# Kernel optimization log

Measured on AMD Instinct MI355X. Metric: run time of the kernel, lower is better.

The kernel has to match this reference:

```python
import jax, jax.numpy as jnp
import numpy as np

B, N, C = 16, 2048, 3           # images, proposals/image, classes (incl. background)
K = 100                         # num_detections kept per class
SCORE_THRESH = 0.05
NMS_THRESH = 0.5
MIN_ANGLE = 10.0                # process_box min width (self.min_angle)
WX, WW = 1.0, 1.0               # box_coder reg_weights
NEG = jnp.float32(-1e9)


def setup_inputs() -> dict:
    key = jax.random.key(0)
    k1, k2, k3, k4 = jax.random.split(key, 4)
    class_logit = jax.random.normal(k1, (B, N, C), jnp.float32)
    box_regression = jax.random.normal(k2, (B, N, 2 * C), jnp.float32) * 0.1
    starts = jax.random.uniform(k3, (B, N), dtype=jnp.float32) * 300.0
    widths = jax.random.uniform(k4, (B, N), dtype=jnp.float32) * 50.0 + 12.0
    proposal = jnp.stack([starts, starts + widths], axis=-1)  # [B,N,2] 1-D intervals
    return {"class_logit": class_logit, "box_regression": box_regression,
            "proposal": proposal, "image_shape": 360}


def _decode(delta, prop):
    w = prop[:, 1] - prop[:, 0]
    ctr = prop[:, 0] + 0.5 * w
    dx = delta[:, 0] / WX
    dw = jnp.minimum(delta[:, 1] / WW, 4.0)  # clamp like torchvision
    pc = dx * w + ctr
    pw = jnp.exp(dw) * w
    return jnp.stack([pc - 0.5 * pw, pc + 0.5 * pw], axis=-1)  # [N,2]


def _iou_1d(a, b):
    inter = jnp.maximum(0.0, jnp.minimum(a[:, None, 1], b[None, :, 1])
                        - jnp.maximum(a[:, None, 0], b[None, :, 0]))
    union = (a[:, None, 1] - a[:, None, 0]) + (b[None, :, 1] - b[None, :, 0]) - inter
    return inter / jnp.maximum(union, 1e-8)  # [Na,Nb]


def _infer_one_class(score, delta, prop, image_shape):
    # score [N], delta [N,2], prop [N,2] -> [K,3] (start, end, score); invalid slots score=NEG
    box = _decode(delta, prop)
    lo = jnp.clip(box[:, 0], 0.0, image_shape)
    hi = jnp.clip(box[:, 1], 0.0, image_shape)
    box = jnp.stack([lo, hi], axis=-1)
    valid = ((hi - lo) >= MIN_ANGLE) & (score >= SCORE_THRESH)
    ms = jnp.where(valid, score, NEG)
    order = jnp.argsort(-ms)
    b = box[order]
    s = ms[order]
    sup = jax.lax.stop_gradient(_iou_1d(b, b)) > NMS_THRESH  # [N,N] bool
    idx = jnp.arange(N)

    def body(keep, i):  # greedy NMS in score order
        kill = sup[i] & keep[i] & (idx > i)
        return keep & ~kill, None

    keep0 = s > 0.5 * NEG
    keep, _ = jax.lax.scan(body, keep0, idx)
    ks = jnp.where(keep, s, NEG)
    top_s, top_i = jax.lax.top_k(ks, K)
    top_b = b[top_i]
    return jnp.concatenate([top_b, top_s[:, None]], axis=-1)  # [K,3]


def reference(class_logit, box_regression, proposal, image_shape):
    img = jnp.float32(image_shape)
    scores = jax.nn.softmax(class_logit, axis=-1)[..., 1:]        # [B,N,C-1] fg classes
    deltas = box_regression.reshape(B, N, C, 2)[:, :, 1:]         # [B,N,C-1,2]
    scores = jnp.moveaxis(scores, -1, 1)                          # [B,C-1,N]
    deltas = jnp.moveaxis(deltas, 2, 1)                           # [B,C-1,N,2]
    f = jax.vmap(jax.vmap(_infer_one_class, in_axes=(0, 0, None, None)),
                 in_axes=(0, 0, 0, None))
    return f(scores, deltas, proposal, img)  # [B, C-1, K, 3]
```

## Files before the change

kernel.cpp:

```cpp
#include <hip/hip_runtime.h>
#include <math.h>

#define B_IMG 16
#define N_PROP 2048
#define C_CLS 3
#define K_OUT 100
#define NTHREADS 1024
#define NWAVES (NTHREADS / 64)
#define NBLK64 (N_PROP / 64)

__device__ __forceinline__ unsigned long long shfl_xor_u64(unsigned long long v, int lx) {
    unsigned int lo = (unsigned int)__shfl_xor((int)(unsigned int)(v & 0xffffffffull), lx, 64);
    unsigned int hi = (unsigned int)__shfl_xor((int)(unsigned int)(v >> 32), lx, 64);
    return ((unsigned long long)hi << 32) | (unsigned long long)lo;
}
__device__ __forceinline__ float readlane_f(float v, int l) {
    return __int_as_float(__builtin_amdgcn_readlane(__float_as_int(v), l));
}
__device__ __forceinline__ unsigned long long readlane_u64(unsigned long long v, int l) {
    unsigned int lo = (unsigned int)__builtin_amdgcn_readlane((int)(unsigned int)(v & 0xffffffffull), l);
    unsigned int hi = (unsigned int)__builtin_amdgcn_readlane((int)(unsigned int)(v >> 32), l);
    return ((unsigned long long)hi << 32) | (unsigned long long)lo;
}
__device__ __forceinline__ bool iou_gt_half(float inter, float uni) {
    double b = (double)fmaxf(uni, 1e-8f);
    return (double)inter * 2.0 > b * 0x1.000001p0;
}
__device__ __forceinline__ float parse_imgf(int raw) {
    return (raw > 0 && raw < 1000000) ? (float)raw : __int_as_float(raw);
}

__global__ __launch_bounds__(NTHREADS)
void roiheads_fused(const float* __restrict__ class_logit,
                    const float* __restrict__ box_reg,
                    const float* __restrict__ proposal,
                    const int* __restrict__ image_shape_p,
                    float* __restrict__ out)
{
#pragma clang fp contract(off)
    __shared__ unsigned long long skey[N_PROP];
    __shared__ float blo_n[N_PROP], bhi_n[N_PROP];
    __shared__ float slo[N_PROP], shi[N_PROP];
    __shared__ unsigned char keep[N_PROP];
    __shared__ unsigned short alv[2][N_PROP];
    __shared__ float clo[64], chi[64];
    __shared__ unsigned long long sup[64];
    __shared__ unsigned long long kmask[NBLK64];
    __shared__ int wsum[NWAVES];
    __shared__ int sh_nvalid;

    const int tid = threadIdx.x;
    const int lane = tid & 63;
    const int wid = tid >> 6;
    const int img = blockIdx.x >> 1;
    const int cls = blockIdx.x & 1;
    const float imgf = parse_imgf(image_shape_p[0]);

    if (tid == 0) sh_nvalid = 0;

    const int p0 = (wid << 7) | (lane << 1);
    const int p1 = p0 | 1;

    unsigned long long r0 = 0, r1 = 0;
#pragma unroll
    for (int e = 0; e < 2; ++e) {
        const int n = p0 + e;
        const size_t g = (size_t)img * N_PROP + n;
        const float* lg = class_logit + g * C_CLS;
        float l0 = lg[0], l1 = lg[1], l2 = lg[2];
        float mx = fmaxf(l0, fmaxf(l1, l2));
        float e0 = (float)exp((double)(l0 - mx));
        float e1 = (float)exp((double)(l1 - mx));
        float e2 = (float)exp((double)(l2 - mx));
        float denom = (e0 + e1) + e2;
        float score = ((cls == 0) ? e1 : e2) / denom;

        const float* dr = box_reg + g * (2 * C_CLS) + 2 * (cls + 1);
        float dx = dr[0];
        float dw = fminf(dr[1], 4.0f);
        const float* pp = proposal + g * 2;
        float pA = pp[0], pB = pp[1];
        float w = pB - pA;
        float ctr = pA + 0.5f * w;
        float tt = dx * w;
        float pc = tt + ctr;
        float pw = (float)exp((double)dw) * w;
        float half = 0.5f * pw;
        float lo = pc - half;
        float hi = pc + half;
        lo = fminf(fmaxf(lo, 0.0f), imgf);
        hi = fminf(fmaxf(hi, 0.0f), imgf);
        bool valid = ((hi - lo) >= 10.0f) && (score >= 0.05f);
        float ms = valid ? score : -1e9f;
        blo_n[n] = lo;
        bhi_n[n] = hi;
        unsigned int uu = __float_as_uint(ms);
        unsigned int enc = (uu & 0x80000000u) ? ~uu : (uu | 0x80000000u);
        unsigned long long key = ((unsigned long long)enc << 32) |
                                 (unsigned long long)(0xFFFFFFFFu - (unsigned int)n);
        if (e == 0) r0 = key; else r1 = key;
    }

    auto pass_inreg = [&](int k, int j) {
        if (j == 1) {
            bool desc = ((p0 & k) == 0);
            bool sw = desc ? (r0 < r1) : (r0 > r1);
            if (sw) { unsigned long long t = r0; r0 = r1; r1 = t; }
        } else {
            int lx = j >> 1;
            unsigned long long o0 = shfl_xor_u64(r0, lx);
            unsigned long long o1 = shfl_xor_u64(r1, lx);
            bool desc = ((p0 & k) == 0);
            bool lower = ((p0 & j) == 0);
            bool takeMax = (lower == desc);
            r0 = takeMax ? (r0 > o0 ? r0 : o0) : (r0 < o0 ? r0 : o0);
            r1 = takeMax ? (r1 > o1 ? r1 : o1) : (r1 < o1 ? r1 : o1);
        }
    };

    for (int k = 2; k <= 128; k <<= 1)
        for (int j = k >> 1; j >= 1; j >>= 1)
            pass_inreg(k, j);

    for (int k = 256; k <= N_PROP; k <<= 1) {
        skey[p0] = r0; skey[p1] = r1;
        __syncthreads();
        for (int j = k >> 1; j >= 128; j >>= 1) {
            int i = ((tid & ~(j - 1)) << 1) | (tid & (j - 1));
            int part = i | j;
            unsigned long long a = skey[i], b = skey[part];
            bool desc_blk = ((i & k) == 0);
            bool sw = desc_blk ? (a < b) : (a > b);
            if (sw) { skey[i] = b; skey[part] = a; }
            __syncthreads();
        }
        r0 = skey[p0]; r1 = skey[p1];
        for (int j = 64; j >= 1; j >>= 1)
            pass_inreg(k, j);
    }
    skey[p0] = r0; skey[p1] = r1;
    __syncthreads();

    for (int i = tid; i < N_PROP; i += NTHREADS) {
        unsigned long long kk = skey[i];
        unsigned int e = (unsigned int)(kk >> 32);
        unsigned int sb = (e & 0x80000000u) ? (e & 0x7FFFFFFFu) : ~e;
        float s = __uint_as_float(sb);
        unsigned int n = 0xFFFFFFFFu - (unsigned int)(kk & 0xFFFFFFFFull);
        slo[i] = blo_n[n];
        shi[i] = bhi_n[n];
        keep[i] = 0;
        bool v = (s > -5e8f);
        unsigned long long mb = __ballot(v);
        if (lane == 0) atomicAdd(&sh_nvalid, __popcll(mb));
        alv[0][i] = (unsigned short)i;
    }
    __syncthreads();

    int na = sh_nvalid;
    int cur = 0;
    int tk = 0;
    const unsigned long long below = (1ull << lane) - 1ull;

    while (na > 0) {
        const int m = (na < 64) ? na : 64;

        unsigned short cp = alv[cur][lane];
        bool cin = (lane < m);
        float qloc = cin ? slo[cp] : 0.0f;
        float qhic = cin ? shi[cp] : 0.0f;

#pragma unroll
        for (int rr4 = 0; rr4 < 4; ++rr4) {
            int rr = (wid << 2) | rr4;
            unsigned long long row = 0;
            if (rr < m) {
                unsigned short rp = alv[cur][rr];
                float rlo = slo[rp], rhi = shi[rp];
                float inter = fmaxf(fminf(rhi, qhic) - fmaxf(rlo, qloc), 0.0f);
                float uni = (rhi - rlo) + (qhic - qloc) - inter;
                bool kill = cin && (lane > rr) && iou_gt_half(inter, uni);
                row = __ballot(kill);
            }
            if (lane == 0) sup[rr] = row;
        }
        __syncthreads();

        unsigned long long rw = sup[lane];
        unsigned long long A = (m >= 64) ? ~0ull : ((1ull << m) - 1ull);
        unsigned long long kept = 0;
        while (A) {
            int c = __builtin_ctzll(A);
            kept |= (1ull << c);
            A &= ~(readlane_u64(rw, c) | (1ull << c));
        }
        const int cnt = __popcll(kept);

        if (wid == 0) {
            bool alive = cin && ((kept >> lane) & 1ull);
            if (alive) {
                keep[cp] = 1;
                int rank = __popcll(kept & below);
                clo[rank] = qloc; chi[rank] = qhic;
            }
        }
        __syncthreads();
        tk += cnt;
        if (tk >= K_OUT) break;

        float klo = 0.0f, khi = 0.0f;
        if (lane < cnt) { klo = clo[lane]; khi = chi[lane]; }
        int base2 = 0;
        for (int start = 64; start < na; start += NTHREADS) {
            int t2 = start + tid;
            unsigned short qq = 0;
            bool surv = false;
            if (t2 < na) {
                qq = alv[cur][t2];
                float qlo = slo[qq], qhi = shi[qq];
                float qw = qhi - qlo;
                bool dead = false;
                for (int r = 0; r < cnt; ++r) {
                    float cl = readlane_f(klo, r);
                    float ch = readlane_f(khi, r);
                    float inter = fmaxf(fminf(qhi, ch) - fmaxf(qlo, cl), 0.0f);
                    float uni = qw + (ch - cl) - inter;
                    dead |= iou_gt_half(inter, uni);
                }
                surv = !dead;
            }
            unsigned long long mb = __ballot(surv);
            if (lane == 0) wsum[wid] = __popcll(mb);
            __syncthreads();
            int off2 = base2, tot = base2;
            for (int w2 = 0; w2 < NWAVES; ++w2) {
                int c2 = wsum[w2];
                if (w2 < wid) off2 += c2;
                tot += c2;
            }
            if (surv) alv[cur ^ 1][off2 + __popcll(mb & below)] = qq;
            base2 = tot;
            __syncthreads();
        }
        na = base2;
        cur ^= 1;
    }

    for (int blk = wid; blk < NBLK64; blk += NWAVES) {
        bool kk = keep[blk * 64 + lane] != 0;
        unsigned long long mb = __ballot(kk);
        if (lane == 0) kmask[blk] = mb;
    }
    __syncthreads();
    {
        float* outp = out + (((size_t)img * 2 + cls) * K_OUT) * 3;
        for (int blk = wid; blk < NBLK64; blk += NWAVES) {
            int kc = 0, nc = 0, nk = 0;
            for (int b = 0; b < NBLK64; ++b) {
                int pc = __popcll(kmask[b]);
                nk += pc;
                if (b < blk) { kc += pc; nc += 64 - pc; }
            }
            if (kc >= K_OUT && nk + nc >= K_OUT && nc >= K_OUT) continue;
            int p = blk * 64 + lane;
            unsigned long long mb = kmask[blk];
            bool k = (mb >> lane) & 1ull;
            int rk = kc + __popcll(mb & below);
            int rn = nc + __popcll((~mb) & below);
            if (k) {
                if (rk < K_OUT) {
                    unsigned long long kk2 = skey[p];
                    unsigned int e = (unsigned int)(kk2 >> 32);
                    unsigned int sb = (e & 0x80000000u) ? (e & 0x7FFFFFFFu) : ~e;
                    outp[rk * 3 + 0] = slo[p];
                    outp[rk * 3 + 1] = shi[p];
                    outp[rk * 3 + 2] = __uint_as_float(sb);
                }
            } else {
                int oi = nk + rn;
                if (oi < K_OUT) {
                    outp[oi * 3 + 0] = slo[p];
                    outp[oi * 3 + 1] = shi[p];
                    outp[oi * 3 + 2] = -1e9f;
                }
            }
        }
    }
}

extern "C" void kernel_launch(void* const* d_in, const int* in_sizes, int n_in,
                              void* d_out, int out_size, void* d_ws, size_t ws_size,
                              hipStream_t stream) {
    const float* class_logit = (const float*)d_in[0];
    const float* box_reg     = (const float*)d_in[1];
    const float* prop        = (const float*)d_in[2];
    const int*   image_shape = (const int*)d_in[3];
    float* out = (float*)d_out;
    (void)d_ws; (void)ws_size;

    roiheads_fused<<<dim3(B_IMG * 2), dim3(NTHREADS), 0, stream>>>(
        class_logit, box_reg, prop, image_shape, out);
}
```

Measured before the change: 97.16 us.

## Widen NMS candidate chunk from 64 to 128 boxes per round

Greedy NMS now resolves 128 candidates per outer round instead of 64. It builds a 128x128 suppression bitmask across all 16 waves and reads row boxes from registers via readlane instead of shared memory. The serial resolution runs in two 64-bit halves. The goal is fewer outer rounds, and with them fewer block-wide syncs and compaction passes before K boxes are kept. The cost is a longer serial ctz loop and more suppression work per round.

```diff
diff --git a/kernel.cpp b/kernel.cpp
--- a/kernel.cpp
+++ b/kernel.cpp
@@ -8,6 +8,7 @@
 #define NTHREADS 1024
 #define NWAVES (NTHREADS / 64)
 #define NBLK64 (N_PROP / 64)
+#define CHUNK 128
 
 __device__ __forceinline__ unsigned long long shfl_xor_u64(unsigned long long v, int lx) {
     unsigned int lo = (unsigned int)__shfl_xor((int)(unsigned int)(v & 0xffffffffull), lx, 64);
@@ -43,8 +44,8 @@
     __shared__ float slo[N_PROP], shi[N_PROP];
     __shared__ unsigned char keep[N_PROP];
     __shared__ unsigned short alv[2][N_PROP];
-    __shared__ float clo[64], chi[64];
-    __shared__ unsigned long long sup[64];
+    __shared__ float clo[CHUNK], chi[CHUNK];
+    __shared__ unsigned long long sup2[CHUNK][2];
     __shared__ unsigned long long kmask[NBLK64];
     __shared__ int wsum[NWAVES];
     __shared__ int sh_nvalid;
@@ -163,55 +164,87 @@
     const unsigned long long below = (1ull << lane) - 1ull;
 
     while (na > 0) {
-        const int m = (na < 64) ? na : 64;
-
-        unsigned short cp = alv[cur][lane];
-        bool cin = (lane < m);
-        float qloc = cin ? slo[cp] : 0.0f;
-        float qhic = cin ? shi[cp] : 0.0f;
+        const int m = (na < CHUNK) ? na : CHUNK;
+
+        unsigned short cp0 = alv[cur][lane];
+        unsigned short cp1 = alv[cur][64 + lane];
+        bool cin0 = (lane < m);
+        bool cin1 = (64 + lane < m);
+        float q0lo = cin0 ? slo[cp0] : 0.0f;
+        float q0hi = cin0 ? shi[cp0] : 0.0f;
+        float q1lo = cin1 ? slo[cp1] : 0.0f;
+        float q1hi = cin1 ? shi[cp1] : 0.0f;
 
 #pragma unroll
-        for (int rr4 = 0; rr4 < 4; ++rr4) {
-            int rr = (wid << 2) | rr4;
-            unsigned long long row = 0;
-            if (rr < m) {
-                unsigned short rp = alv[cur][rr];
-                float rlo = slo[rp], rhi = shi[rp];
-                float inter = fmaxf(fminf(rhi, qhic) - fmaxf(rlo, qloc), 0.0f);
-                float uni = (rhi - rlo) + (qhic - qloc) - inter;
-                bool kill = cin && (lane > rr) && iou_gt_half(inter, uni);
-                row = __ballot(kill);
-            }
-            if (lane == 0) sup[rr] = row;
+        for (int rr8 = 0; rr8 < 8; ++rr8) {
+            int r = (wid << 3) | rr8;
+            unsigned long long row0 = 0, row1 = 0;
+            if (r < m) {
+                float rlo, rhi;
+                if (wid < 8) { rlo = readlane_f(q0lo, r); rhi = readlane_f(q0hi, r); }
+                else         { rlo = readlane_f(q1lo, r - 64); rhi = readlane_f(q1hi, r - 64); }
+                float rw = rhi - rlo;
+                float inter0 = fmaxf(fminf(rhi, q0hi) - fmaxf(rlo, q0lo), 0.0f);
+                float uni0 = rw + (q0hi - q0lo) - inter0;
+                bool k0 = cin0 && (lane > r) && iou_gt_half(inter0, uni0);
+                row0 = __ballot(k0);
+                bool cgt = (r < 64) ? true : (lane > (r - 64));
+                float inter1 = fmaxf(fminf(rhi, q1hi) - fmaxf(rlo, q1lo), 0.0f);
+                float uni1 = rw + (q1hi - q1lo) - inter1;
+                bool k1 = cin1 && cgt && iou_gt_half(inter1, uni1);
+                row1 = __ballot(k1);
+            }
+            if (lane == 0) { sup2[r][0] = row0; sup2[r][1] = row1; }
         }
         __syncthreads();
 
-        unsigned long long rw = sup[lane];
-        unsigned long long A = (m >= 64) ? ~0ull : ((1ull << m) - 1ull);
-        unsigned long long kept = 0;
-        while (A) {
-            int c = __builtin_ctzll(A);
-            kept |= (1ull << c);
-            A &= ~(readlane_u64(rw, c) | (1ull << c));
-        }
-        const int cnt = __popcll(kept);
+        unsigned long long rA0 = sup2[lane][0];
+        unsigned long long rA1 = sup2[lane][1];
+        unsigned long long rB1 = sup2[64 + lane][1];
+        unsigned long long a0 = (m >= 64) ? ~0ull : ((1ull << m) - 1ull);
+        unsigned long long a1 = (m >= 128) ? ~0ull : ((m > 64) ? ((1ull << (m - 64)) - 1ull) : 0ull);
+        unsigned long long kept0 = 0, kept1 = 0;
+        while (a0) {
+            int c = __builtin_ctzll(a0);
+            unsigned long long b = 1ull << c;
+            kept0 |= b;
+            a0 &= ~(readlane_u64(rA0, c) | b);
+            a1 &= ~readlane_u64(rA1, c);
+        }
+        while (a1) {
+            int c = __builtin_ctzll(a1);
+            unsigned long long b = 1ull << c;
+            kept1 |= b;
+            a1 &= ~(readlane_u64(rB1, c) | b);
+        }
+        const int cnt0 = __popcll(kept0);
+        const int cnt = cnt0 + __popcll(kept1);
 
         if (wid == 0) {
-            bool alive = cin && ((kept >> lane) & 1ull);
+            bool alive = cin0 && ((kept0 >> lane) & 1ull);
             if (alive) {
-                keep[cp] = 1;
-                int rank = __popcll(kept & below);
-                clo[rank] = qloc; chi[rank] = qhic;
+                keep[cp0] = 1;
+                int rank = __popcll(kept0 & below);
+                clo[rank] = q0lo; chi[rank] = q0hi;
+            }
+        } else if (wid == 1) {
+            bool alive = cin1 && ((kept1 >> lane) & 1ull);
+            if (alive) {
+                keep[cp1] = 1;
+                int rank = cnt0 + __popcll(kept1 & below);
+                clo[rank] = q1lo; chi[rank] = q1hi;
             }
         }
         __syncthreads();
         tk += cnt;
         if (tk >= K_OUT) break;
 
-        float klo = 0.0f, khi = 0.0f;
-        if (lane < cnt) { klo = clo[lane]; khi = chi[lane]; }
+        float klo0 = 0.0f, khi0 = 0.0f, klo1 = 0.0f, khi1 = 0.0f;
+        if (lane < cnt) { klo0 = clo[lane]; khi0 = chi[lane]; }
+        if (64 + lane < cnt) { klo1 = clo[64 + lane]; khi1 = chi[64 + lane]; }
+        const int c0n = (cnt < 64) ? cnt : 64;
         int base2 = 0;
-        for (int start = 64; start < na; start += NTHREADS) {
+        for (int start = CHUNK; start < na; start += NTHREADS) {
             int t2 = start + tid;
             unsigned short qq = 0;
             bool surv = false;
@@ -220,9 +253,16 @@
                 float qlo = slo[qq], qhi = shi[qq];
                 float qw = qhi - qlo;
                 bool dead = false;
-                for (int r = 0; r < cnt; ++r) {
-                    float cl = readlane_f(klo, r);
-                    float ch = readlane_f(khi, r);
+                for (int r = 0; r < c0n; ++r) {
+                    float cl = readlane_f(klo0, r);
+                    float ch = readlane_f(khi0, r);
+                    float inter = fmaxf(fminf(qhi, ch) - fmaxf(qlo, cl), 0.0f);
+                    float uni = qw + (ch - cl) - inter;
+                    dead |= iou_gt_half(inter, uni);
+                }
+                for (int r = 64; r < cnt; ++r) {
+                    float cl = readlane_f(klo1, r - 64);
+                    float ch = readlane_f(khi1, r - 64);
                     float inter = fmaxf(fminf(qhi, ch) - fmaxf(qlo, cl), 0.0f);
                     float uni = qw + (ch - cl) - inter;
                     dead |= iou_gt_half(inter, uni);
```

Measured after the change: 105.0 us. 1.08x slower.

## Replace block-wide iterative NMS compaction with single-wave chunked greedy NMS

Applied to the files above, without the earlier changes.

Greedy NMS no longer uses the whole 1024-thread block. Before, each round built a 64x64 suppression matrix, did a block-wide compaction of survivors, and needed several __syncthreads per round. Now one wave walks the sorted boxes in chunks of 64, tests each chunk against the kept list held in shared memory, then resolves the chunk internally with ballots. This removes the block barriers and the survivor compaction, at the cost of serialising the work on a single wave while the other waves sit idle.

```diff
diff --git a/kernel.cpp b/kernel.cpp
--- a/kernel.cpp
+++ b/kernel.cpp
@@ -8,6 +8,8 @@
 #define NTHREADS 1024
 #define NWAVES (NTHREADS / 64)
 #define NBLK64 (N_PROP / 64)
+#define KEPT_MAX 192
+
 
 __device__ __forceinline__ unsigned long long shfl_xor_u64(unsigned long long v, int lx) {
     unsigned int lo = (unsigned int)__shfl_xor((int)(unsigned int)(v & 0xffffffffull), lx, 64);
@@ -16,11 +18,6 @@
 }
 __device__ __forceinline__ float readlane_f(float v, int l) {
     return __int_as_float(__builtin_amdgcn_readlane(__float_as_int(v), l));
-}
-__device__ __forceinline__ unsigned long long readlane_u64(unsigned long long v, int l) {
-    unsigned int lo = (unsigned int)__builtin_amdgcn_readlane((int)(unsigned int)(v & 0xffffffffull), l);
-    unsigned int hi = (unsigned int)__builtin_amdgcn_readlane((int)(unsigned int)(v >> 32), l);
-    return ((unsigned long long)hi << 32) | (unsigned long long)lo;
 }
 __device__ __forceinline__ bool iou_gt_half(float inter, float uni) {
     double b = (double)fmaxf(uni, 1e-8f);
@@ -42,11 +39,8 @@
     __shared__ float blo_n[N_PROP], bhi_n[N_PROP];
     __shared__ float slo[N_PROP], shi[N_PROP];
     __shared__ unsigned char keep[N_PROP];
-    __shared__ unsigned short alv[2][N_PROP];
-    __shared__ float clo[64], chi[64];
-    __shared__ unsigned long long sup[64];
+    __shared__ float clo[KEPT_MAX], chi[KEPT_MAX];
     __shared__ unsigned long long kmask[NBLK64];
-    __shared__ int wsum[NWAVES];
     __shared__ int sh_nvalid;
 
     const int tid = threadIdx.x;
@@ -60,6 +54,7 @@
 
     const int p0 = (wid << 7) | (lane << 1);
     const int p1 = p0 | 1;
+    const unsigned long long below = (1ull << lane) - 1ull;
 
     unsigned long long r0 = 0, r1 = 0;
 #pragma unroll
@@ -153,98 +148,48 @@
         bool v = (s > -5e8f);
         unsigned long long mb = __ballot(v);
         if (lane == 0) atomicAdd(&sh_nvalid, __popcll(mb));
-        alv[0][i] = (unsigned short)i;
-    }
-    __syncthreads();
-
-    int na = sh_nvalid;
-    int cur = 0;
-    int tk = 0;
-    const unsigned long long below = (1ull << lane) - 1ull;
-
-    while (na > 0) {
-        const int m = (na < 64) ? na : 64;
-
-        unsigned short cp = alv[cur][lane];
-        bool cin = (lane < m);
-        float qloc = cin ? slo[cp] : 0.0f;
-        float qhic = cin ? shi[cp] : 0.0f;
-
-#pragma unroll
-        for (int rr4 = 0; rr4 < 4; ++rr4) {
-            int rr = (wid << 2) | rr4;
-            unsigned long long row = 0;
-            if (rr < m) {
-                unsigned short rp = alv[cur][rr];
-                float rlo = slo[rp], rhi = shi[rp];
-                float inter = fmaxf(fminf(rhi, qhic) - fmaxf(rlo, qloc), 0.0f);
-                float uni = (rhi - rlo) + (qhic - qloc) - inter;
-                bool kill = cin && (lane > rr) && iou_gt_half(inter, uni);
-                row = __ballot(kill);
-            }
-            if (lane == 0) sup[rr] = row;
-        }
-        __syncthreads();
-
-        unsigned long long rw = sup[lane];
-        unsigned long long A = (m >= 64) ? ~0ull : ((1ull << m) - 1ull);
-        unsigned long long kept = 0;
-        while (A) {
-            int c = __builtin_ctzll(A);
-            kept |= (1ull << c);
-            A &= ~(readlane_u64(rw, c) | (1ull << c));
-        }
-        const int cnt = __popcll(kept);
-
-        if (wid == 0) {
-            bool alive = cin && ((kept >> lane) & 1ull);
-            if (alive) {
-                keep[cp] = 1;
-                int rank = __popcll(kept & below);
-                clo[rank] = qloc; chi[rank] = qhic;
-            }
-        }
-        __syncthreads();
-        tk += cnt;
-        if (tk >= K_OUT) break;
-
-        float klo = 0.0f, khi = 0.0f;
-        if (lane < cnt) { klo = clo[lane]; khi = chi[lane]; }
-        int base2 = 0;
-        for (int start = 64; start < na; start += NTHREADS) {
-            int t2 = start + tid;
-            unsigned short qq = 0;
-            bool surv = false;
-            if (t2 < na) {
-                qq = alv[cur][t2];
-                float qlo = slo[qq], qhi = shi[qq];
-                float qw = qhi - qlo;
-                bool dead = false;
-                for (int r = 0; r < cnt; ++r) {
-                    float cl = readlane_f(klo, r);
-                    float ch = readlane_f(khi, r);
-                    float inter = fmaxf(fminf(qhi, ch) - fmaxf(qlo, cl), 0.0f);
-                    float uni = qw + (ch - cl) - inter;
-                    dead |= iou_gt_half(inter, uni);
-                }
-                surv = !dead;
-            }
-            unsigned long long mb = __ballot(surv);
-            if (lane == 0) wsum[wid] = __popcll(mb);
-            __syncthreads();
-            int off2 = base2, tot = base2;
-            for (int w2 = 0; w2 < NWAVES; ++w2) {
-                int c2 = wsum[w2];
-                if (w2 < wid) off2 += c2;
-                tot += c2;
-            }
-            if (surv) alv[cur ^ 1][off2 + __popcll(mb & below)] = qq;
-            base2 = tot;
-            __syncthreads();
-        }
-        na = base2;
-        cur ^= 1;
-    }
+    }
+    __syncthreads();
+
+    const int nvalid = sh_nvalid;
+
+    if (wid == 0) {
+        int tk = 0;
+        for (int c0 = 0; c0 < nvalid && tk < K_OUT; c0 += 64) {
+            const int p = c0 + lane;
+            const bool in = (p < nvalid);
+            float qlo = in ? slo[p] : 0.0f;
+            float qhi = in ? shi[p] : 0.0f;
+            bool alive = in;
+            for (int r = 0; r < tk; ++r) {
+                float cl = clo[r], ch = chi[r];
+                float inter = fmaxf(fminf(ch, qhi) - fmaxf(cl, qlo), 0.0f);
+                float uni = (ch - cl) + (qhi - qlo) - inter;
+                alive = alive && !iou_gt_half(inter, uni);
+                if (__ballot(alive) == 0ull) break;
+            }
+            unsigned long long A = __ballot(alive);
+            unsigned long long kept = 0;
+            while (A) {
+                int c = __builtin_ctzll(A);
+                unsigned long long bit = 1ull << c;
+                kept |= bit;
+                float rlo = readlane_f(qlo, c);
+                float rhi = readlane_f(qhi, c);
+                float inter = fmaxf(fminf(rhi, qhi) - fmaxf(rlo, qlo), 0.0f);
+                float uni = (rhi - rlo) + (qhi - qlo) - inter;
+                bool kill = (lane > c) && iou_gt_half(inter, uni);
+                A &= ~(__ballot(kill) | bit);
+            }
+            if ((kept >> lane) & 1ull) {
+                keep[p] = 1;
+                int rank = tk + __popcll(kept & below);
+                clo[rank] = qlo; chi[rank] = qhi;
+            }
+            tk += __popcll(kept);
+        }
+    }
+    __syncthreads();
 
     for (int blk = wid; blk < NBLK64; blk += NWAVES) {
         bool kk = keep[blk * 64 + lane] != 0;
```

After: 263.0 us. 171% more time.

## Flatten NMS suppression pass to two fixed items per thread with early prefetch

Applied to the files above, without the earlier changes.

Replaces the strided loop over the remaining candidate list with exactly two candidates per thread (N=2048 fits in 1024 threads x 2), loading them before the first barrier so the LDS reads overlap the 64x64 suppression-matrix build. A single packed per-wave count and one barrier pair do the compaction instead of two barriers per chunk. The IoU test now uses a float fast path and falls back to double only near the threshold, and the kept boxes are stored as float2 read directly from LDS instead of via readlane. Correctness relies on na never exceeding 64+2048, and the float prefilter has to stay exactly consistent with the double comparison.

```diff
diff --git a/kernel.cpp b/kernel.cpp
--- a/kernel.cpp
+++ b/kernel.cpp
@@ -9,6 +9,7 @@
 #define NWAVES (NTHREADS / 64)
 #define NBLK64 (N_PROP / 64)
 
+
 __device__ __forceinline__ unsigned long long shfl_xor_u64(unsigned long long v, int lx) {
     unsigned int lo = (unsigned int)__shfl_xor((int)(unsigned int)(v & 0xffffffffull), lx, 64);
     unsigned int hi = (unsigned int)__shfl_xor((int)(unsigned int)(v >> 32), lx, 64);
@@ -23,8 +24,14 @@
     return ((unsigned long long)hi << 32) | (unsigned long long)lo;
 }
 __device__ __forceinline__ bool iou_gt_half(float inter, float uni) {
-    double b = (double)fmaxf(uni, 1e-8f);
-    return (double)inter * 2.0 > b * 0x1.000001p0;
+    float b = fmaxf(uni, 1e-8f);
+    float lhs = 2.0f * inter;
+    if (__builtin_expect(lhs > b, 0)) {
+        if (lhs > b * 0x1.000004p0f) return true;
+        double bb = (double)b;
+        return (double)inter * 2.0 > bb * 0x1.000001p0;
+    }
+    return false;
 }
 __device__ __forceinline__ float parse_imgf(int raw) {
     return (raw > 0 && raw < 1000000) ? (float)raw : __int_as_float(raw);
@@ -43,7 +50,7 @@
     __shared__ float slo[N_PROP], shi[N_PROP];
     __shared__ unsigned char keep[N_PROP];
     __shared__ unsigned short alv[2][N_PROP];
-    __shared__ float clo[64], chi[64];
+    __shared__ float2 cbox[64];
     __shared__ unsigned long long sup[64];
     __shared__ unsigned long long kmask[NBLK64];
     __shared__ int wsum[NWAVES];
@@ -60,6 +67,7 @@
 
     const int p0 = (wid << 7) | (lane << 1);
     const int p1 = p0 | 1;
+    const unsigned long long below = (1ull << lane) - 1ull;
 
     unsigned long long r0 = 0, r1 = 0;
 #pragma unroll
@@ -160,7 +168,6 @@
     int na = sh_nvalid;
     int cur = 0;
     int tk = 0;
-    const unsigned long long below = (1ull << lane) - 1ull;
 
     while (na > 0) {
         const int m = (na < 64) ? na : 64;
@@ -184,6 +191,17 @@
             }
             if (lane == 0) sup[rr] = row;
         }
+
+        const int iA = 64 + tid;
+        const int iB = 64 + NTHREADS + tid;
+        const bool vA = (iA < na);
+        const bool vB = (iB < na);
+        unsigned short qqA = vA ? alv[cur][iA] : 0;
+        unsigned short qqB = vB ? alv[cur][iB] : 0;
+        float qAlo = vA ? slo[qqA] : 0.0f;
+        float qAhi = vA ? shi[qqA] : 0.0f;
+        float qBlo = vB ? slo[qqB] : 0.0f;
+        float qBhi = vB ? shi[qqB] : 0.0f;
         __syncthreads();
 
         unsigned long long rw = sup[lane];
@@ -201,48 +219,47 @@
             if (alive) {
                 keep[cp] = 1;
                 int rank = __popcll(kept & below);
-                clo[rank] = qloc; chi[rank] = qhic;
+                cbox[rank] = make_float2(qloc, qhic);
             }
         }
         __syncthreads();
         tk += cnt;
         if (tk >= K_OUT) break;
 
-        float klo = 0.0f, khi = 0.0f;
-        if (lane < cnt) { klo = clo[lane]; khi = chi[lane]; }
-        int base2 = 0;
-        for (int start = 64; start < na; start += NTHREADS) {
-            int t2 = start + tid;
-            unsigned short qq = 0;
-            bool surv = false;
-            if (t2 < na) {
-                qq = alv[cur][t2];
-                float qlo = slo[qq], qhi = shi[qq];
-                float qw = qhi - qlo;
-                bool dead = false;
-                for (int r = 0; r < cnt; ++r) {
-                    float cl = readlane_f(klo, r);
-                    float ch = readlane_f(khi, r);
-                    float inter = fmaxf(fminf(qhi, ch) - fmaxf(qlo, cl), 0.0f);
-                    float uni = qw + (ch - cl) - inter;
-                    dead |= iou_gt_half(inter, uni);
-                }
-                surv = !dead;
-            }
-            unsigned long long mb = __ballot(surv);
-            if (lane == 0) wsum[wid] = __popcll(mb);
-            __syncthreads();
-            int off2 = base2, tot = base2;
-            for (int w2 = 0; w2 < NWAVES; ++w2) {
-                int c2 = wsum[w2];
-                if (w2 < wid) off2 += c2;
-                tot += c2;
-            }
-            if (surv) alv[cur ^ 1][off2 + __popcll(mb & below)] = qq;
-            base2 = tot;
-            __syncthreads();
-        }
-        na = base2;
+        bool survA = vA, survB = vB;
+        {
+            float qAw = qAhi - qAlo;
+            float qBw = qBhi - qBlo;
+            bool dA = false, dB = false;
+#pragma unroll 4
+            for (int r = 0; r < cnt; ++r) {
+                float2 cb = cbox[r];
+                float interA = fmaxf(fminf(qAhi, cb.y) - fmaxf(qAlo, cb.x), 0.0f);
+                float uniA = qAw + (cb.y - cb.x) - interA;
+                dA |= iou_gt_half(interA, uniA);
+                float interB = fmaxf(fminf(qBhi, cb.y) - fmaxf(qBlo, cb.x), 0.0f);
+                float uniB = qBw + (cb.y - cb.x) - interB;
+                dB |= iou_gt_half(interB, uniB);
+            }
+            survA = vA && !dA;
+            survB = vB && !dB;
+        }
+        unsigned long long mbA = __ballot(survA);
+        unsigned long long mbB = __ballot(survB);
+        if (lane == 0) wsum[wid] = (__popcll(mbA) << 16) | __popcll(mbB);
+        __syncthreads();
+        int offA = 0, offB = 0, totA = 0, totB = 0;
+#pragma unroll
+        for (int w2 = 0; w2 < NWAVES; ++w2) {
+            unsigned pk = (unsigned)wsum[w2];
+            int ca = (int)(pk >> 16), cb2 = (int)(pk & 0xffffu);
+            if (w2 < wid) { offA += ca; offB += cb2; }
+            totA += ca; totB += cb2;
+        }
+        if (survA) alv[cur ^ 1][offA + __popcll(mbA & below)] = qqA;
+        if (survB) alv[cur ^ 1][totA + offB + __popcll(mbB & below)] = qqB;
+        __syncthreads();
+        na = totA + totB;
         cur ^= 1;
     }
 
```

Result: slower. 109.5 us (+12.7%).
